# Optimization experiments

Hardware: AMD Instinct MI355X
Metric: run time of the kernel (lower is better)

Reference implementation:

```python
import jax, jax.numpy as jnp
import numpy as np

B, T, D = 4, 4096, 1024

def setup_inputs() -> dict:
    key = jax.random.key(0)
    ks = jax.random.split(key, 8)
    s = 1.0 / np.sqrt(D)
    return {
        "x": jax.random.normal(ks[0], (B, T, D), dtype=jnp.float32),
        # diagonal SSM params (per-channel)
        "A": jax.random.uniform(ks[1], (D,), dtype=jnp.float32, minval=0.5, maxval=0.99),  # stable decay
        "Bp": jax.random.normal(ks[2], (D,), dtype=jnp.float32) * 0.1,
        "Cp": jax.random.normal(ks[3], (D,), dtype=jnp.float32),
        # gate Linear
        "gate_w": jax.random.uniform(ks[4], (D, D), dtype=jnp.float32, minval=-s, maxval=s),
        "gate_b": jnp.zeros((D,), dtype=jnp.float32),
        # out Linear
        "out_w": jax.random.uniform(ks[5], (D, D), dtype=jnp.float32, minval=-s, maxval=s),
        "out_b": jnp.zeros((D,), dtype=jnp.float32),
    }

def _ssm(x, A, Bp, Cp):
    # diagonal linear recurrence: h_t = A*h_{t-1} + Bp*x_t ; y_t = Cp*h_t
    bx = x * Bp  # (B,T,D)
    def step(h, bx_t):
        h = A * h + bx_t  # (B,D)
        return h, h
    h0 = jnp.zeros((x.shape[0], x.shape[2]), dtype=x.dtype)
    _, hs = jax.lax.scan(step, h0, jnp.swapaxes(bx, 0, 1))  # (T,B,D)
    return jnp.swapaxes(hs, 0, 1) * Cp  # (B,T,D)

def reference(x, A, Bp, Cp, gate_w, gate_b, out_w, out_b):
    ssm_out = _ssm(x, A, Bp, Cp)
    gate = jax.nn.sigmoid(jnp.einsum('btd,ed->bte', x, gate_w) + gate_b)
    y = gate * ssm_out
    return jnp.einsum('btd,ed->bte', y, out_w) + out_b
```

## Files before the change

### kernel.cpp

```cpp
#include <hip/hip_runtime.h>
#include <hip/hip_bf16.h>
#include <cstdio>

typedef __hip_bfloat16 bf16;
typedef __bf16 bf16x8 __attribute__((ext_vector_type(8)));
typedef float f32x4 __attribute__((ext_vector_type(4)));

#define B_DIM 4
#define T_DIM 4096
#define D_DIM 1024
#define NC 64
#define LC 64

#define M_DIM (B_DIM * T_DIM)
#define BM 128
#define BN 256
#define BK 32
#define NT (D_DIM / BK)
#define GM (M_DIM / BM)
#define GN (D_DIM / BN)

__global__ __launch_bounds__(256) void cast_w_kernel(
    const float* __restrict__ gw, const float* __restrict__ ow,
    bf16* __restrict__ gw16, bf16* __restrict__ ow16, int n) {
  int i = blockIdx.x * 256 + threadIdx.x;
  if (i < n) {
    gw16[i] = __float2bfloat16(gw[i]);
    ow16[i] = __float2bfloat16(ow[i]);
  }
}

__global__ __launch_bounds__(256) void ssm_pass1(
    const float* __restrict__ x, const float* __restrict__ A,
    const float* __restrict__ Bp, float* __restrict__ hfin) {
  const int tid  = threadIdx.x;
  const int dblk = blockIdx.x & 3;
  const int c    = (blockIdx.x >> 2) & (NC - 1);
  const int b    = blockIdx.x >> 8;
  const int d    = dblk * 256 + tid;
  const float a = A[d], bp = Bp[d];
  const float* p = x + ((size_t)(b * T_DIM + c * LC) * D_DIM + d);
  float h = 0.f;
#pragma unroll 4
  for (int i = 0; i < LC; ++i)
    h = fmaf(a, h, bp * p[(size_t)i * D_DIM]);
  hfin[(b * NC + c) * D_DIM + d] = h;
}

__global__ __launch_bounds__(256) void ssm_pass2(
    const float* __restrict__ A, const float* __restrict__ hfin,
    float* __restrict__ hin) {
  const int idx = blockIdx.x * 256 + threadIdx.x;
  const int d = idx & (D_DIM - 1);
  const int b = idx >> 10;
  float aL = A[d];
#pragma unroll
  for (int s = 0; s < 6; ++s) aL *= aL;
  float h = 0.f;
  for (int c = 0; c < NC; ++c) {
    const int o = (b * NC + c) * D_DIM + d;
    hin[o] = h;
    h = fmaf(aL, h, hfin[o]);
  }
}

__global__ __launch_bounds__(256) void ssm_pass3(
    const float* __restrict__ x, const float* __restrict__ A,
    const float* __restrict__ Bp, const float* __restrict__ Cp,
    const float* __restrict__ hin, bf16* __restrict__ ssm16,
    bf16* __restrict__ x16) {
  const int tid  = threadIdx.x;
  const int dblk = blockIdx.x & 3;
  const int c    = (blockIdx.x >> 2) & (NC - 1);
  const int b    = blockIdx.x >> 8;
  const int d    = dblk * 256 + tid;
  const float a = A[d], bp = Bp[d], cp = Cp[d];
  float h = hin[(b * NC + c) * D_DIM + d];
  const size_t base = (size_t)(b * T_DIM + c * LC) * D_DIM + d;
#pragma unroll 4
  for (int i = 0; i < LC; ++i) {
    const size_t o = base + (size_t)i * D_DIM;
    const float xv = x[o];
    h = fmaf(a, h, bp * xv);
    ssm16[o] = __float2bfloat16(cp * h);
    x16[o]  = __float2bfloat16(xv);
  }
}

template <bool GATE>
__global__ __launch_bounds__(256, 2) void gemm128(
    const bf16* __restrict__ Xm, const bf16* __restrict__ Wm,
    const float* __restrict__ bias, const bf16* __restrict__ ssm,
    bf16* __restrict__ Ybf, float* __restrict__ Yf) {
  __shared__ __align__(16) short LDS[3][12288];

  const int tid  = threadIdx.x;
  const int lane = tid & 63;
  const int wave = tid >> 6;
  const int l15 = lane & 15;
  const int sA = ((lane >> 4) ^ ((l15 >> 1) & 3)) << 3;

  const int bid = blockIdx.x;
  const int swz = (bid & 7) * (GM * GN / 8) + (bid >> 3);
  const int m0 = (swz >> 2) * BM;
  const int n0 = (swz & 3) * BN;

  const int row0 = tid >> 2;
  const int c0   = (tid & 3) ^ ((row0 >> 1) & 3);
  size_t offA[2], offB[4];
#pragma unroll
  for (int it = 0; it < 2; ++it)
    offA[it] = (size_t)(m0 + it * 64 + row0) * D_DIM + c0 * 8;
#pragma unroll
  for (int it = 0; it < 4; ++it)
    offB[it] = (size_t)(n0 + it * 64 + row0) * D_DIM + c0 * 8;

  auto gll = [](const bf16* g, short* l) {
    __builtin_amdgcn_global_load_lds(
        (const __attribute__((address_space(1))) void*)g,
        (__attribute__((address_space(3))) void*)l, 16, 0, 0);
  };
  auto STAGE = [&](int buf, int kt) {
    const size_t ko = (size_t)kt * BK;
#pragma unroll
    for (int it = 0; it < 2; ++it)
      gll(Xm + offA[it] + ko, &LDS[buf][(it * 256 + wave * 64) * 8]);
#pragma unroll
    for (int it = 0; it < 4; ++it)
      gll(Wm + offB[it] + ko, &LDS[buf][4096 + (it * 256 + wave * 64) * 8]);
  };

  f32x4 acc[8][4] = {};

  STAGE(0, 0);
  STAGE(1, 1);
  asm volatile("s_waitcnt vmcnt(6)" ::: "memory");
  __builtin_amdgcn_s_barrier();

#define KTILE_BODY(RB_, SB_, KT2_, VMSTR, DO_STAGE, DO_BAR)                 \
  {                                                                         \
    const short* bb = &LDS[RB_][0];                                         \
    bf16x8 a[8], b[4];                                                      \
    _Pragma("unroll")                                                       \
    for (int i = 0; i < 8; ++i)                                             \
      a[i] = *(const bf16x8*)(bb + (i * 16 + l15) * BK + sA);               \
    _Pragma("unroll")                                                       \
    for (int j = 0; j < 4; ++j)                                             \
      b[j] = *(const bf16x8*)(bb + 4096 + (wave * 64 + j * 16 + l15) * BK + sA); \
    if (DO_STAGE) STAGE(SB_, KT2_);                                         \
    asm volatile("s_waitcnt lgkmcnt(0)" ::: "memory");                      \
    __builtin_amdgcn_sched_barrier(0);                                      \
    __builtin_amdgcn_s_setprio(1);                                          \
    _Pragma("unroll")                                                       \
    for (int i = 0; i < 4; ++i)                                             \
      _Pragma("unroll")                                                     \
      for (int j = 0; j < 4; ++j)                                           \
        acc[i][j] =                                                         \
            __builtin_amdgcn_mfma_f32_16x16x32_bf16(a[i], b[j], acc[i][j], 0, 0, 0); \
    __builtin_amdgcn_s_setprio(0);                                          \
    if (DO_BAR) {                                                           \
      asm volatile("s_waitcnt " VMSTR ::: "memory");                        \
      __builtin_amdgcn_s_barrier();                                         \
    }                                                                       \
    __builtin_amdgcn_s_setprio(1);                                          \
    _Pragma("unroll")                                                       \
    for (int i = 4; i < 8; ++i)                                             \
      _Pragma("unroll")                                                     \
      for (int j = 0; j < 4; ++j)                                           \
        acc[i][j] =                                                         \
            __builtin_amdgcn_mfma_f32_16x16x32_bf16(a[i], b[j], acc[i][j], 0, 0, 0); \
    __builtin_amdgcn_s_setprio(0);                                          \
  }

  {
    int rb = 0;
    for (int t = 0; t < NT - 2; ++t) {
      int sb = rb + 2; if (sb >= 3) sb -= 3;
      KTILE_BODY(rb, sb, t + 2, "vmcnt(6)", true, true);
      ++rb; if (rb == 3) rb = 0;
    }
  }
  KTILE_BODY((NT - 2) % 3, 0, 0, "vmcnt(0)", false, true);
  KTILE_BODY((NT - 1) % 3, 0, 0, "vmcnt(0)", false, false);
#undef KTILE_BODY

#pragma unroll
  for (int i = 0; i < 8; ++i) {
#pragma unroll
    for (int j = 0; j < 4; ++j) {
      const int col = n0 + wave * 64 + j * 16 + l15;
      const float bv = bias[col];
#pragma unroll
      for (int v = 0; v < 4; ++v) {
        const int row = m0 + i * 16 + (lane >> 4) * 4 + v;
        const size_t o = (size_t)row * D_DIM + col;
        const float val = acc[i][j][v] + bv;
        if (GATE) {
          const float g = 1.f / (1.f + expf(-val));
          Ybf[o] = __float2bfloat16(g * __bfloat162float(ssm[o]));
        } else {
          Yf[o] = val;
        }
      }
    }
  }
}

extern "C" void kernel_launch(void* const* d_in, const int* in_sizes, int n_in,
                              void* d_out, int out_size, void* d_ws, size_t ws_size,
                              hipStream_t stream) {
  const float* x  = (const float*)d_in[0];
  const float* A  = (const float*)d_in[1];
  const float* Bp = (const float*)d_in[2];
  const float* Cp = (const float*)d_in[3];
  const float* gw = (const float*)d_in[4];
  const float* gb = (const float*)d_in[5];
  const float* ow = (const float*)d_in[6];
  const float* ob = (const float*)d_in[7];
  float* out = (float*)d_out;

  const size_t NEED = 73400320;
  if (ws_size < NEED) {
    fprintf(stderr, "kernel_launch: ws_size %zu < needed %zu\n", ws_size, NEED);
    return;
  }
  char* ws = (char*)d_ws;
  bf16*  x16   = (bf16*)(ws);
  bf16*  ssm16 = (bf16*)(ws + 33554432);
  bf16*  gw16  = (bf16*)(ws + 67108864);
  bf16*  ow16  = (bf16*)(ws + 69206016);
  float* hfin  = (float*)(ws + 71303168);
  float* hin   = (float*)(ws + 72351744);

  cast_w_kernel<<<(D_DIM * D_DIM) / 256, 256, 0, stream>>>(gw, ow, gw16, ow16, D_DIM * D_DIM);
  ssm_pass1<<<B_DIM * NC * (D_DIM / 256), 256, 0, stream>>>(x, A, Bp, hfin);
  ssm_pass2<<<(B_DIM * D_DIM) / 256, 256, 0, stream>>>(A, hfin, hin);
  ssm_pass3<<<B_DIM * NC * (D_DIM / 256), 256, 0, stream>>>(x, A, Bp, Cp, hin, ssm16, x16);

  gemm128<true><<<GM * GN, 256, 0, stream>>>(x16, gw16, gb, ssm16, ssm16, nullptr);
  gemm128<false><<<GM * GN, 256, 0, stream>>>(ssm16, ow16, ob, nullptr, nullptr, out);
}
```

Baseline: 137.0 us.

## Reshape GEMM block to 256x128 tile with eight waves in a 4x2 grid

The two bf16 MFMA GEMMs change from a 128x256 tile run by 4 waves to a 256x128 tile run by 512 threads (8 waves arranged 4x2). Each wave now owns a 64x64 sub-tile, so it holds half the accumulators, and each thread issues three global-to-LDS loads per stage instead of six. The explicit lgkmcnt(0) wait and the sched_barrier before the MFMAs are removed, and launch bounds are raised to (512,4). The aim is more waves per CU for latency hiding. The risk is that the tighter register budget implied by the new launch bounds causes spills, and that the 72KB LDS footprint per block still limits occupancy.

```diff
diff --git a/kernel.cpp b/kernel.cpp
--- a/kernel.cpp
+++ b/kernel.cpp
@@ -13,8 +13,8 @@
 #define LC 64
 
 #define M_DIM (B_DIM * T_DIM)
-#define BM 128
-#define BN 256
+#define BM 256
+#define BN 128
 #define BK 32
 #define NT (D_DIM / BK)
 #define GM (M_DIM / BM)
@@ -88,7 +88,7 @@
 }
 
 template <bool GATE>
-__global__ __launch_bounds__(256, 2) void gemm128(
+__global__ __launch_bounds__(512, 4) void gemm256(
     const bf16* __restrict__ Xm, const bf16* __restrict__ Wm,
     const float* __restrict__ bias, const bf16* __restrict__ ssm,
     bf16* __restrict__ Ybf, float* __restrict__ Yf) {
@@ -97,23 +97,21 @@
   const int tid  = threadIdx.x;
   const int lane = tid & 63;
   const int wave = tid >> 6;
+  const int wr = wave >> 1;
+  const int wc = wave & 1;
   const int l15 = lane & 15;
   const int sA = ((lane >> 4) ^ ((l15 >> 1) & 3)) << 3;
 
   const int bid = blockIdx.x;
   const int swz = (bid & 7) * (GM * GN / 8) + (bid >> 3);
-  const int m0 = (swz >> 2) * BM;
-  const int n0 = (swz & 3) * BN;
+  const int m0 = (swz >> 3) * BM;
+  const int n0 = (swz & 7) * BN;
 
   const int row0 = tid >> 2;
   const int c0   = (tid & 3) ^ ((row0 >> 1) & 3);
-  size_t offA[2], offB[4];
-#pragma unroll
-  for (int it = 0; it < 2; ++it)
-    offA[it] = (size_t)(m0 + it * 64 + row0) * D_DIM + c0 * 8;
-#pragma unroll
-  for (int it = 0; it < 4; ++it)
-    offB[it] = (size_t)(n0 + it * 64 + row0) * D_DIM + c0 * 8;
+  const size_t offA0 = (size_t)(m0 + row0) * D_DIM + c0 * 8;
+  const size_t offA1 = offA0 + (size_t)128 * D_DIM;
+  const size_t offB0 = (size_t)(n0 + row0) * D_DIM + c0 * 8;
 
   auto gll = [](const bf16* g, short* l) {
     __builtin_amdgcn_global_load_lds(
@@ -122,39 +120,35 @@
   };
   auto STAGE = [&](int buf, int kt) {
     const size_t ko = (size_t)kt * BK;
-#pragma unroll
-    for (int it = 0; it < 2; ++it)
-      gll(Xm + offA[it] + ko, &LDS[buf][(it * 256 + wave * 64) * 8]);
-#pragma unroll
-    for (int it = 0; it < 4; ++it)
-      gll(Wm + offB[it] + ko, &LDS[buf][4096 + (it * 256 + wave * 64) * 8]);
+    short* b0 = &LDS[buf][0] + wave * 512;
+    gll(Xm + offA0 + ko, b0);
+    gll(Xm + offA1 + ko, b0 + 4096);
+    gll(Wm + offB0 + ko, b0 + 8192);
   };
 
-  f32x4 acc[8][4] = {};
+  f32x4 acc[4][4] = {};
 
   STAGE(0, 0);
   STAGE(1, 1);
-  asm volatile("s_waitcnt vmcnt(6)" ::: "memory");
+  asm volatile("s_waitcnt vmcnt(3)" ::: "memory");
   __builtin_amdgcn_s_barrier();
 
 #define KTILE_BODY(RB_, SB_, KT2_, VMSTR, DO_STAGE, DO_BAR)                 \
   {                                                                         \
     const short* bb = &LDS[RB_][0];                                         \
-    bf16x8 a[8], b[4];                                                      \
-    _Pragma("unroll")                                                       \
-    for (int i = 0; i < 8; ++i)                                             \
-      a[i] = *(const bf16x8*)(bb + (i * 16 + l15) * BK + sA);               \
+    bf16x8 a[4], b[4];                                                      \
+    _Pragma("unroll")                                                       \
+    for (int i = 0; i < 4; ++i)                                             \
+      a[i] = *(const bf16x8*)(bb + (wr * 64 + i * 16 + l15) * BK + sA);     \
     _Pragma("unroll")                                                       \
     for (int j = 0; j < 4; ++j)                                             \
-      b[j] = *(const bf16x8*)(bb + 4096 + (wave * 64 + j * 16 + l15) * BK + sA); \
+      b[j] = *(const bf16x8*)(bb + 8192 + (wc * 64 + j * 16 + l15) * BK + sA); \
     if (DO_STAGE) STAGE(SB_, KT2_);                                         \
-    asm volatile("s_waitcnt lgkmcnt(0)" ::: "memory");                      \
-    __builtin_amdgcn_sched_barrier(0);                                      \
     __builtin_amdgcn_s_setprio(1);                                          \
     _Pragma("unroll")                                                       \
     for (int i = 0; i < 4; ++i)                                             \
       _Pragma("unroll")                                                     \
-      for (int j = 0; j < 4; ++j)                                           \
+      for (int j = 0; j < 2; ++j)                                           \
         acc[i][j] =                                                         \
             __builtin_amdgcn_mfma_f32_16x16x32_bf16(a[i], b[j], acc[i][j], 0, 0, 0); \
     __builtin_amdgcn_s_setprio(0);                                          \
@@ -164,9 +158,9 @@
     }                                                                       \
     __builtin_amdgcn_s_setprio(1);                                          \
     _Pragma("unroll")                                                       \
-    for (int i = 4; i < 8; ++i)                                             \
+    for (int i = 0; i < 4; ++i)                                             \
       _Pragma("unroll")                                                     \
-      for (int j = 0; j < 4; ++j)                                           \
+      for (int j = 2; j < 4; ++j)                                           \
         acc[i][j] =                                                         \
             __builtin_amdgcn_mfma_f32_16x16x32_bf16(a[i], b[j], acc[i][j], 0, 0, 0); \
     __builtin_amdgcn_s_setprio(0);                                          \
@@ -176,7 +170,7 @@
     int rb = 0;
     for (int t = 0; t < NT - 2; ++t) {
       int sb = rb + 2; if (sb >= 3) sb -= 3;
-      KTILE_BODY(rb, sb, t + 2, "vmcnt(6)", true, true);
+      KTILE_BODY(rb, sb, t + 2, "vmcnt(3)", true, true);
       ++rb; if (rb == 3) rb = 0;
     }
   }
@@ -185,14 +179,14 @@
 #undef KTILE_BODY
 
 #pragma unroll
-  for (int i = 0; i < 8; ++i) {
+  for (int i = 0; i < 4; ++i) {
 #pragma unroll
     for (int j = 0; j < 4; ++j) {
-      const int col = n0 + wave * 64 + j * 16 + l15;
+      const int col = n0 + wc * 64 + j * 16 + l15;
       const float bv = bias[col];
 #pragma unroll
       for (int v = 0; v < 4; ++v) {
-        const int row = m0 + i * 16 + (lane >> 4) * 4 + v;
+        const int row = m0 + wr * 64 + i * 16 + (lane >> 4) * 4 + v;
         const size_t o = (size_t)row * D_DIM + col;
         const float val = acc[i][j][v] + bv;
         if (GATE) {
@@ -237,6 +231,6 @@
   ssm_pass2<<<(B_DIM * D_DIM) / 256, 256, 0, stream>>>(A, hfin, hin);
   ssm_pass3<<<B_DIM * NC * (D_DIM / 256), 256, 0, stream>>>(x, A, Bp, Cp, hin, ssm16, x16);
 
-  gemm128<true><<<GM * GN, 256, 0, stream>>>(x16, gw16, gb, ssm16, ssm16, nullptr);
-  gemm128<false><<<GM * GN, 256, 0, stream>>>(ssm16, ow16, ob, nullptr, nullptr, out);
-}
+  gemm256<true><<<GM * GN, 512, 0, stream>>>(x16, gw16, gb, ssm16, ssm16, nullptr);
+  gemm256<false><<<GM * GN, 512, 0, stream>>>(ssm16, ow16, ob, nullptr, nullptr, out);
+}
```

After: 134.5 us. About the same (-1.8%).
